# Performance work log

Measured on AMD Instinct MI355X. Metric: run time of the kernel, lower is better.

Reference implementation:

```python
import jax, jax.numpy as jnp
import numpy as np

QLEN, BSZ, D_MODEL = 2048, 4, 1024
N_HEAD, D_HEAD = 16, 64
SCALE = 1.0 / D_HEAD ** 0.5


def _rope(t, cos, sin):
    # t: [len, b, n, d_head]; cos/sin: [len, d_head//2]
    tr = t.reshape(*t.shape[:-1], D_HEAD // 2, 2)
    t_r, t_i = tr[..., 0], tr[..., 1]
    c = cos[:, None, None, :]
    s = sin[:, None, None, :]
    o_r = t_r * c - t_i * s
    o_i = t_r * s + t_i * c
    return jnp.stack([o_r, o_i], axis=-1).reshape(t.shape)


def setup_inputs() -> dict:
    key = jax.random.key(0)
    ks = jax.random.split(key, 9)
    x = jax.random.normal(ks[0], (QLEN, BSZ, D_MODEL), dtype=jnp.float32)
    # standard RoPE frequencies: theta = 10000^{-2i/d_head}
    inv_freq = 1.0 / (10000.0 ** (np.arange(0, D_HEAD, 2, dtype=np.float32) / D_HEAD))
    ang = np.arange(QLEN, dtype=np.float32)[:, None] * inv_freq[None, :]
    freqs_cos = jnp.asarray(np.cos(ang))
    freqs_sin = jnp.asarray(np.sin(ang))
    init = lambda k, sh: (jax.random.normal(k, sh, dtype=jnp.float32) * 0.02)
    H = N_HEAD * D_HEAD
    return {
        "x": x,
        "freqs_cos": freqs_cos,
        "freqs_sin": freqs_sin,
        "Wq": init(ks[1], (D_MODEL, H)), "bq": jnp.zeros((H,), jnp.float32),
        "Wk": init(ks[2], (D_MODEL, H)), "bk": jnp.zeros((H,), jnp.float32),
        "Wv": init(ks[3], (D_MODEL, H)), "bv": jnp.zeros((H,), jnp.float32),
        "Wo": init(ks[4], (H, D_MODEL)), "bo": jnp.zeros((D_MODEL,), jnp.float32),
    }


def reference(x, freqs_cos, freqs_sin, Wq, bq, Wk, bk, Wv, bv, Wo, bo):
    qlen, bsz, _ = x.shape
    q = x @ Wq + bq  # [q, b, n*d]
    k = x @ Wk + bk
    v = x @ Wv + bv
    new_mem = (k, v)
    q = q.reshape(qlen, bsz, N_HEAD, D_HEAD)
    k = k.reshape(qlen, bsz, N_HEAD, D_HEAD)
    vv = v.reshape(qlen, bsz, N_HEAD, D_HEAD)
    q = _rope(q, freqs_cos, freqs_sin)
    k = _rope(k, freqs_cos, freqs_sin)
    attn = jnp.einsum('ibnd,jbnd->ijbn', q, k) * SCALE
    p = jax.nn.softmax(attn, axis=1)
    o = jnp.einsum('ijbn,jbnd->ibnd', p, vv)
    o = o.reshape(qlen, bsz, N_HEAD * D_HEAD) @ Wo + bo
    return (o, new_mem[0], new_mem[1])
```

## Files before the change

kernel.cpp:

```cpp
#include <hip/hip_runtime.h>

typedef __attribute__((ext_vector_type(4))) float f32x4;
typedef __attribute__((ext_vector_type(16))) float f32x16;
typedef __attribute__((ext_vector_type(8))) __bf16 bf16x8;
typedef __attribute__((ext_vector_type(4))) __bf16 bf16x4;
typedef __attribute__((ext_vector_type(2))) __bf16 bf16x2;
typedef __attribute__((ext_vector_type(8))) unsigned short ushort8;
typedef __attribute__((ext_vector_type(4))) unsigned int u32x4;

#define DEVI __device__ __forceinline__

static constexpr int QLEN = 2048, BSZ = 4, DM = 1024, NH = 16, DH = 64;
static constexpr int MROWS = QLEN * BSZ;
static constexpr long OSZ  = (long)MROWS * DM;
static constexpr float SCL2E = 0.125f * 1.4426950408889634f;
static constexpr float RAW_THR = 4.0f / SCL2E;

DEVI void gload_lds16(const void* g, void* l) {
  __builtin_amdgcn_global_load_lds(
      (__attribute__((address_space(1))) void*)(size_t)g,
      (__attribute__((address_space(3))) void*)l, 16, 0, 0);
}

DEVI f32x16 zero16() {
  f32x16 v;
#pragma unroll
  for (int i = 0; i < 16; ++i) v[i] = 0.f;
  return v;
}

DEVI unsigned pack_bf16(float lo, float hi) {
  bf16x2 v = { (__bf16)lo, (__bf16)hi };
  return __builtin_bit_cast(unsigned, v);
}

__global__ void k_f32_to_bf16(const float* __restrict__ in, __bf16* __restrict__ out, int n4) {
  int i = blockIdx.x * blockDim.x + threadIdx.x;
  int stride = gridDim.x * blockDim.x;
  for (; i < n4; i += stride) {
    const float4 v = ((const float4*)in)[i];
    bf16x4 o = { (__bf16)v.x, (__bf16)v.y, (__bf16)v.z, (__bf16)v.w };
    ((bf16x4*)out)[i] = o;
  }
}

__global__ void k_wtrans(const float* __restrict__ W, __bf16* __restrict__ Wt) {
  __shared__ float tile[64][65];
  const int tk = blockIdx.x >> 4;
  const int tn = blockIdx.x & 15;
  const int t = threadIdx.x;
  const int r = t >> 4;
  const int c4 = (t & 15) << 2;
#pragma unroll
  for (int i = 0; i < 4; ++i) {
    const float4 v = *(const float4*)&W[(size_t)(tk * 64 + r + i * 16) * DM + tn * 64 + c4];
    tile[r + i * 16][c4 + 0] = v.x;
    tile[r + i * 16][c4 + 1] = v.y;
    tile[r + i * 16][c4 + 2] = v.z;
    tile[r + i * 16][c4 + 3] = v.w;
  }
  __syncthreads();
#pragma unroll
  for (int i = 0; i < 4; ++i) {
    const int n = r + i * 16;
    bf16x4 o = { (__bf16)tile[c4 + 0][n], (__bf16)tile[c4 + 1][n],
                 (__bf16)tile[c4 + 2][n], (__bf16)tile[c4 + 3][n] };
    *(bf16x4*)&Wt[(size_t)(tn * 64 + n) * DM + tk * 64 + c4] = o;
  }
}

DEVI void gemm_tile_core(const __bf16* __restrict__ A, const __bf16* __restrict__ Bt,
                         char* Alds, char* Blds, int m0, int n0, int t,
                         f32x4 (&acc)[4][4]) {
  constexpr int K = 1024;
  const int l = t & 63;
  const int w = t >> 6;
  const int wr = w >> 1, wc = w & 1;

  int a_addr[2][4], b_addr[2][4];
#pragma unroll
  for (int s = 0; s < 2; ++s)
#pragma unroll
    for (int f = 0; f < 4; ++f) {
      const int ca = s * 64 + ((l >> 4) << 4);
      const int ra = wr * 64 + f * 16 + (l & 15);
      a_addr[s][f] = ra * 128 + (ca ^ ((ra & 7) << 4));
      const int rb = wc * 64 + f * 16 + (l & 15);
      b_addr[s][f] = rb * 128 + (ca ^ ((rb & 7) << 4));
    }

  int g_row[4], g_col[4];
#pragma unroll
  for (int i = 0; i < 4; ++i) {
    const int g = i * 256 + t;
    g_row[i] = g >> 3;
    g_col[i] = ((g & 7) ^ (g_row[i] & 7)) * 8;
  }

  for (int kt = 0; kt < K / 64; ++kt) {
#pragma unroll
    for (int i = 0; i < 4; ++i) {
      gload_lds16(A + (size_t)(m0 + g_row[i]) * K + kt * 64 + g_col[i],
                  Alds + (size_t)(i * 256 + t) * 16);
      gload_lds16(Bt + (size_t)(n0 + g_row[i]) * K + kt * 64 + g_col[i],
                  Blds + (size_t)(i * 256 + t) * 16);
    }
    __syncthreads();
#pragma unroll
    for (int s = 0; s < 2; ++s) {
      bf16x8 af[4], bfr[4];
#pragma unroll
      for (int f = 0; f < 4; ++f) {
        af[f]  = *(const bf16x8*)(Alds + a_addr[s][f]);
        bfr[f] = *(const bf16x8*)(Blds + b_addr[s][f]);
      }
#pragma unroll
      for (int mi = 0; mi < 4; ++mi)
#pragma unroll
        for (int ni = 0; ni < 4; ++ni)
          acc[mi][ni] = __builtin_amdgcn_mfma_f32_16x16x32_bf16(af[mi], bfr[ni], acc[mi][ni], 0, 0, 0);
    }
    __syncthreads();
  }
}

__global__ __launch_bounds__(256, 2) void k_gemm(
    const __bf16* __restrict__ A, const __bf16* __restrict__ Bt,
    const float* __restrict__ bias, float* __restrict__ Cf, __bf16* __restrict__ Cb) {
  __shared__ alignas(16) char lds[32768];
  const int t = threadIdx.x;
  const int l = t & 63;
  const int w = t >> 6;
  const int n0 = (blockIdx.x & 7) * 128;
  const int m0 = (blockIdx.x >> 3) * 128;
  const int wr = w >> 1, wc = w & 1;

  f32x4 acc[4][4];
#pragma unroll
  for (int i = 0; i < 4; ++i)
#pragma unroll
    for (int j = 0; j < 4; ++j) acc[i][j] = (f32x4){0.f, 0.f, 0.f, 0.f};

  gemm_tile_core(A, Bt, lds, lds + 16384, m0, n0, t, acc);

  const int rowb = m0 + wr * 64 + ((l >> 4) << 2);
  const int colb = n0 + wc * 64 + (l & 15);
#pragma unroll
  for (int ni = 0; ni < 4; ++ni) {
    const float bv = bias[colb + ni * 16];
#pragma unroll
    for (int mi = 0; mi < 4; ++mi)
#pragma unroll
      for (int r = 0; r < 4; ++r) {
        const float v = acc[mi][ni][r] + bv;
        const size_t idx = (size_t)(rowb + mi * 16 + r) * 1024 + colb + ni * 16;
        Cf[idx] = v;
        if (Cb) Cb[idx] = (__bf16)v;
      }
  }
}

__global__ __launch_bounds__(256, 2) void k_gemm_qkv(
    const __bf16* __restrict__ A, const __bf16* __restrict__ Bt,
    const float* __restrict__ bq, const float* __restrict__ bk, const float* __restrict__ bv,
    float* __restrict__ oq, float* __restrict__ ok, float* __restrict__ ov,
    __bf16* __restrict__ vb) {
  __shared__ alignas(16) char lds[32768];
  const int t = threadIdx.x;
  const int l = t & 63;
  const int w = t >> 6;
  const int nt = blockIdx.x % 24;
  const int n0 = nt * 128;
  const int m0 = (blockIdx.x / 24) * 128;
  const int wr = w >> 1, wc = w & 1;

  f32x4 acc[4][4];
#pragma unroll
  for (int i = 0; i < 4; ++i)
#pragma unroll
    for (int j = 0; j < 4; ++j) acc[i][j] = (f32x4){0.f, 0.f, 0.f, 0.f};

  gemm_tile_core(A, Bt, lds, lds + 16384, m0, n0, t, acc);

  const int grp = n0 >> 10;
  const float* bias = grp == 0 ? bq : (grp == 1 ? bk : bv);
  float* Cf = grp == 0 ? oq : (grp == 1 ? ok : ov);
  __bf16* Cb = grp == 2 ? vb : nullptr;

  const int rowb = m0 + wr * 64 + ((l >> 4) << 2);
  const int colb = (n0 & 1023) + wc * 64 + (l & 15);
#pragma unroll
  for (int ni = 0; ni < 4; ++ni) {
    const float bvv = bias[colb + ni * 16];
#pragma unroll
    for (int mi = 0; mi < 4; ++mi)
#pragma unroll
      for (int r = 0; r < 4; ++r) {
        const float v = acc[mi][ni][r] + bvv;
        const size_t idx = (size_t)(rowb + mi * 16 + r) * 1024 + colb + ni * 16;
        Cf[idx] = v;
        if (Cb) Cb[idx] = (__bf16)v;
      }
  }
}

__global__ void k_rope(const float* __restrict__ qf, const float* __restrict__ kf,
                       const float* __restrict__ fc, const float* __restrict__ fs,
                       __bf16* __restrict__ qr, __bf16* __restrict__ kr) {
  const int i = blockIdx.x * blockDim.x + threadIdx.x;
  const int m = i >> 8;
  const int cp2 = i & 255;
  const int s = m >> 2;
  const int p2 = cp2 & 15;
  const float2 c2 = *(const float2*)&fc[s * 32 + p2 * 2];
  const float2 s2 = *(const float2*)&fs[s * 32 + p2 * 2];
  const float4 q4 = ((const float4*)qf)[i];
  const float4 k4 = ((const float4*)kf)[i];
  bf16x4 qo = { (__bf16)(q4.x * c2.x - q4.y * s2.x), (__bf16)(q4.x * s2.x + q4.y * c2.x),
                (__bf16)(q4.z * c2.y - q4.w * s2.y), (__bf16)(q4.z * s2.y + q4.w * c2.y) };
  bf16x4 ko = { (__bf16)(k4.x * c2.x - k4.y * s2.x), (__bf16)(k4.x * s2.x + k4.y * c2.x),
                (__bf16)(k4.z * c2.y - k4.w * s2.y), (__bf16)(k4.z * s2.y + k4.w * c2.y) };
  ((bf16x4*)qr)[i] = qo;
  ((bf16x4*)kr)[i] = ko;
}

static constexpr int KSLAB = 8192;
static constexpr int VSLAB_STRIDE = 1040;
static constexpr int VSLAB = 8 * VSLAB_STRIDE;
static constexpr int FBUF = KSLAB + VSLAB;

__global__ __launch_bounds__(256, 4) void k_flash3(
    const __bf16* __restrict__ Q, const __bf16* __restrict__ Kr,
    const __bf16* __restrict__ V, __bf16* __restrict__ O) {
  __shared__ alignas(16) char lds[2 * FBUF];

  const int t = threadIdx.x, l = t & 63, w = t >> 6;
  const int hf = l >> 5;
  const int q32 = l & 31;
  const int bid = blockIdx.x;
  const int qt = bid & 15;
  const int bh = bid >> 4;
  const int b = bh >> 4, hd = bh & 15;

  const int qrow = qt * 128 + w * 32 + q32;

  bf16x8 qf[4];
#pragma unroll
  for (int kc = 0; kc < 4; ++kc)
    qf[kc] = *(const bf16x8*)(Q + (size_t)(qrow * 4 + b) * DM + hd * 64 + kc * 16 + hf * 8);

  f32x16 acc0 = zero16(), acc1 = zero16();
  float m_run = -3.0e38f, l_run = 0.f;

  const int ksrc_j = t & 31;
  const int ksrc_d = (t >> 5) * 8;

  const int vj0 = (t & 31) * 2;
  const int vd0 = (t >> 5) * 8;
  const int vt_wbase = ((((t & 31) >> 3) * 2 + (t >> 7)) * VSLAB_STRIDE)
                     + (((((t & 31) >> 2) & 1) * 32 + (((t >> 5) & 3) * 8)) * 16)
                     + (((t & 31) & 3) * 4);

  {
    char* Kl = lds;
#pragma unroll
    for (int i = 0; i < 2; ++i)
      gload_lds16(Kr + (size_t)(((0 * 64) + i * 32 + ksrc_j) * 4 + b) * DM + hd * 64 + ksrc_d,
                  Kl + (size_t)(i * 256 + t) * 16);
    const __bf16* vsrc = V + (size_t)((0 * 64 + vj0) * 4 + b) * DM + hd * 64 + vd0;
    const ushort8 r0 = *(const ushort8*)vsrc;
    const ushort8 r1 = *(const ushort8*)(vsrc + 4 * DM);
    char* Vl = lds + KSLAB;
#pragma unroll
    for (int e = 0; e < 8; ++e) {
      const unsigned pack = (unsigned)r0[e] | ((unsigned)r1[e] << 16);
      *(unsigned*)(Vl + vt_wbase + e * 16) = pack;
    }
  }

  for (int kt = 0; kt < QLEN / 64; ++kt) {
    const int cur = kt & 1;
    char* Kl = lds + cur * FBUF;
    char* Vl = Kl + KSLAB;
    char* Kn = lds + (cur ^ 1) * FBUF;
    char* Vn = Kn + KSLAB;

    __syncthreads();

    ushort8 vr0, vr1;
    const bool have_next = (kt + 1) < QLEN / 64;
    if (have_next) {
#pragma unroll
      for (int i = 0; i < 2; ++i)
        gload_lds16(Kr + (size_t)((((kt + 1) * 64) + i * 32 + ksrc_j) * 4 + b) * DM + hd * 64 + ksrc_d,
                    Kn + (size_t)(i * 256 + t) * 16);
      const __bf16* vsrc = V + (size_t)(((kt + 1) * 64 + vj0) * 4 + b) * DM + hd * 64 + vd0;
      vr0 = *(const ushort8*)vsrc;
      vr1 = *(const ushort8*)(vsrc + 4 * DM);
    }

#pragma unroll
    for (int c = 0; c < 2; ++c) {
      f32x16 sc = zero16();
#pragma unroll
      for (int kc = 0; kc < 4; ++kc) {
        const bf16x8 kf = *(const bf16x8*)(Kl + (c * 4 + kc) * 1024 + l * 16);
        sc = __builtin_amdgcn_mfma_f32_32x32x16_bf16(kf, qf[kc], sc, 0, 0, 0);
      }

      float red[8];
#pragma unroll
      for (int i = 0; i < 8; ++i) red[i] = fmaxf(sc[i], sc[i + 8]);
#pragma unroll
      for (int i = 0; i < 4; ++i) red[i] = fmaxf(red[i], red[i + 4]);
      float pmax = fmaxf(fmaxf(red[0], red[2]), fmaxf(red[1], red[3]));
      pmax = fmaxf(pmax, __shfl_xor(pmax, 32));

      if (!__all(pmax - m_run <= RAW_THR)) {
        const float mn = fmaxf(m_run, pmax);
        const float alpha = __builtin_amdgcn_exp2f((m_run - mn) * SCL2E);
        l_run *= alpha;
        acc0 = acc0 * alpha;
        acc1 = acc1 * alpha;
        m_run = mn;
      }

#pragma unroll
      for (int r = 0; r < 16; ++r) sc[r] = __builtin_amdgcn_exp2f((sc[r] - m_run) * SCL2E);
      float sred[8];
#pragma unroll
      for (int i = 0; i < 8; ++i) sred[i] = sc[i] + sc[i + 8];
#pragma unroll
      for (int i = 0; i < 4; ++i) sred[i] = sred[i] + sred[i + 4];
      float rs = (sred[0] + sred[2]) + (sred[1] + sred[3]);
      rs += __shfl_xor(rs, 32);
      l_run += rs;

      unsigned pk[8];
#pragma unroll
      for (int m = 0; m < 4; ++m)
#pragma unroll
        for (int i = 0; i < 2; ++i)
          pk[m * 2 + i] = pack_bf16(sc[4 * m + 2 * i], sc[4 * m + 2 * i + 1]);

#pragma unroll
      for (int jc2 = 0; jc2 < 2; ++jc2) {
        unsigned w0 = pk[4 * jc2 + 0], w2 = pk[4 * jc2 + 2];
        unsigned w1 = pk[4 * jc2 + 1], w3 = pk[4 * jc2 + 3];
        asm("v_permlane32_swap_b32 %0, %1" : "+v"(w0), "+v"(w2));
        asm("v_permlane32_swap_b32 %0, %1" : "+v"(w1), "+v"(w3));
        const u32x4 pw = { w0, w1, w2, w3 };
        const bf16x8 pf = __builtin_bit_cast(bf16x8, pw);
        const int jc = c * 2 + jc2;
        {
          const bf16x8 vf = *(const bf16x8*)(Vl + (jc * 2 + 0) * VSLAB_STRIDE + l * 16);
          acc0 = __builtin_amdgcn_mfma_f32_32x32x16_bf16(vf, pf, acc0, 0, 0, 0);
        }
        {
          const bf16x8 vf = *(const bf16x8*)(Vl + (jc * 2 + 1) * VSLAB_STRIDE + l * 16);
          acc1 = __builtin_amdgcn_mfma_f32_32x32x16_bf16(vf, pf, acc1, 0, 0, 0);
        }
      }
    }

    if (have_next) {
#pragma unroll
      for (int e = 0; e < 8; ++e) {
        const unsigned pack = (unsigned)vr0[e] | ((unsigned)vr1[e] << 16);
        *(unsigned*)(Vn + vt_wbase + e * 16) = pack;
      }
    }
  }

  const float inv = 1.0f / l_run;
#pragma unroll
  for (int g = 0; g < 4; ++g) {
    {
      const int d0 = 0 * 32 + 8 * g + 4 * hf;
      bf16x4 o4 = { (__bf16)(acc0[4 * g + 0] * inv), (__bf16)(acc0[4 * g + 1] * inv),
                    (__bf16)(acc0[4 * g + 2] * inv), (__bf16)(acc0[4 * g + 3] * inv) };
      *(bf16x4*)&O[(size_t)(qrow * 4 + b) * DM + hd * 64 + d0] = o4;
    }
    {
      const int d0 = 1 * 32 + 8 * g + 4 * hf;
      bf16x4 o4 = { (__bf16)(acc1[4 * g + 0] * inv), (__bf16)(acc1[4 * g + 1] * inv),
                    (__bf16)(acc1[4 * g + 2] * inv), (__bf16)(acc1[4 * g + 3] * inv) };
      *(bf16x4*)&O[(size_t)(qrow * 4 + b) * DM + hd * 64 + d0] = o4;
    }
  }
}

extern "C" void kernel_launch(void* const* d_in, const int* in_sizes, int n_in,
                              void* d_out, int out_size, void* d_ws, size_t ws_size,
                              hipStream_t stream) {
  const float* x    = (const float*)d_in[0];
  const float* fcos = (const float*)d_in[1];
  const float* fsin = (const float*)d_in[2];
  const float* Wq   = (const float*)d_in[3];
  const float* bq   = (const float*)d_in[4];
  const float* Wk   = (const float*)d_in[5];
  const float* bk   = (const float*)d_in[6];
  const float* Wv   = (const float*)d_in[7];
  const float* bv   = (const float*)d_in[8];
  const float* Wo   = (const float*)d_in[9];
  const float* bo   = (const float*)d_in[10];

  float* out_o = (float*)d_out;
  float* out_k = out_o + OSZ;
  float* out_v = out_o + 2 * OSZ;

  char* ws = (char*)d_ws;
  __bf16* xb  = (__bf16*)(ws);
  __bf16* wqt = (__bf16*)(ws + 16777216);
  __bf16* wkt = (__bf16*)(ws + 18874368);
  __bf16* wvt = (__bf16*)(ws + 20971520);
  __bf16* wot = (__bf16*)(ws + 23068672);
  __bf16* qr  = (__bf16*)(ws + 25165824);
  __bf16* kr  = (__bf16*)(ws + 41943040);
  __bf16* vb  = (__bf16*)(ws + 58720256);
  __bf16* ao  = (__bf16*)(ws + 75497472);

  k_f32_to_bf16<<<2048, 256, 0, stream>>>(x, xb, (int)(OSZ / 4));
  k_wtrans<<<256, 256, 0, stream>>>(Wq, wqt);
  k_wtrans<<<256, 256, 0, stream>>>(Wk, wkt);
  k_wtrans<<<256, 256, 0, stream>>>(Wv, wvt);
  k_wtrans<<<256, 256, 0, stream>>>(Wo, wot);

  k_gemm_qkv<<<1536, 256, 0, stream>>>(xb, wqt, bq, bk, bv, out_o, out_k, out_v, vb);

  k_rope<<<8192, 256, 0, stream>>>(out_o, out_k, fcos, fsin, qr, kr);

  k_flash3<<<1024, 256, 0, stream>>>(qr, kr, vb, ao);

  k_gemm<<<512, 256, 0, stream>>>(ao, wot, bo, out_o, (__bf16*)nullptr);
}
```

Before: 226.8 us.

## Fuse RoPE into QKV GEMM epilogue, pre-transpose V, add MFMA priority hints

RoPE is now applied in the QKV GEMM epilogue using a lane shuffle to fetch the paired element. This removes the separate rope kernel and the fp32 Q round trip through the output buffer. A new kernel transposes V into a per-head [d, seq] layout, reusing the xb workspace, so the flash kernel reads V fragments straight from global memory instead of staging transposed tiles in LDS. The change also adds s_setprio around MFMA blocks, a swizzled block order, and a cheaper max reduction. In exchange it adds an extra launch and V pass, and flash now issues uncached global V loads inside the loop.

Result: slower. 276.8 us (+22.1%).

```diff
diff --git a/kernel.cpp b/kernel.cpp
--- a/kernel.cpp
+++ b/kernel.cpp
@@ -69,6 +69,33 @@
   }
 }
 
+__global__ __launch_bounds__(256, 4) void k_vtrans(const __bf16* __restrict__ vb,
+                                                   __bf16* __restrict__ VT) {
+  __shared__ __bf16 tile[128][66];
+  const int t = threadIdx.x;
+  const int bh = blockIdx.x >> 4;
+  const int s0 = (blockIdx.x & 15) * 128;
+  const int b = bh >> 4, h = bh & 15;
+  const int sl = t >> 4;
+  const int d4 = (t & 15) * 4;
+#pragma unroll
+  for (int it = 0; it < 8; ++it) {
+    const int s = sl + it * 16;
+    *(bf16x4*)&tile[s][d4] = *(const bf16x4*)&vb[(size_t)((s0 + s) * 4 + b) * DM + h * 64 + d4];
+  }
+  __syncthreads();
+  const int d = t >> 2;
+  const int sp = t & 3;
+#pragma unroll
+  for (int j = 0; j < 4; ++j) {
+    const int sb = sp * 32 + j * 8;
+    bf16x8 pk;
+#pragma unroll
+    for (int i = 0; i < 8; ++i) pk[i] = tile[sb + i][d];
+    *(bf16x8*)&VT[(size_t)(bh * 64 + d) * QLEN + s0 + sb] = pk;
+  }
+}
+
 DEVI void gemm_tile_core(const __bf16* __restrict__ A, const __bf16* __restrict__ Bt,
                          char* Alds, char* Blds, int m0, int n0, int t,
                          f32x4 (&acc)[4][4]) {
@@ -114,11 +141,13 @@
         af[f]  = *(const bf16x8*)(Alds + a_addr[s][f]);
         bfr[f] = *(const bf16x8*)(Blds + b_addr[s][f]);
       }
+      __builtin_amdgcn_s_setprio(1);
 #pragma unroll
       for (int mi = 0; mi < 4; ++mi)
 #pragma unroll
         for (int ni = 0; ni < 4; ++ni)
           acc[mi][ni] = __builtin_amdgcn_mfma_f32_16x16x32_bf16(af[mi], bfr[ni], acc[mi][ni], 0, 0, 0);
+      __builtin_amdgcn_s_setprio(0);
     }
     __syncthreads();
   }
@@ -126,7 +155,7 @@
 
 __global__ __launch_bounds__(256, 2) void k_gemm(
     const __bf16* __restrict__ A, const __bf16* __restrict__ Bt,
-    const float* __restrict__ bias, float* __restrict__ Cf, __bf16* __restrict__ Cb) {
+    const float* __restrict__ bias, float* __restrict__ Cf) {
   __shared__ alignas(16) char lds[32768];
   const int t = threadIdx.x;
   const int l = t & 63;
@@ -151,20 +180,17 @@
 #pragma unroll
     for (int mi = 0; mi < 4; ++mi)
 #pragma unroll
-      for (int r = 0; r < 4; ++r) {
-        const float v = acc[mi][ni][r] + bv;
-        const size_t idx = (size_t)(rowb + mi * 16 + r) * 1024 + colb + ni * 16;
-        Cf[idx] = v;
-        if (Cb) Cb[idx] = (__bf16)v;
-      }
+      for (int r = 0; r < 4; ++r)
+        Cf[(size_t)(rowb + mi * 16 + r) * 1024 + colb + ni * 16] = acc[mi][ni][r] + bv;
   }
 }
 
 __global__ __launch_bounds__(256, 2) void k_gemm_qkv(
     const __bf16* __restrict__ A, const __bf16* __restrict__ Bt,
     const float* __restrict__ bq, const float* __restrict__ bk, const float* __restrict__ bv,
-    float* __restrict__ oq, float* __restrict__ ok, float* __restrict__ ov,
-    __bf16* __restrict__ vb) {
+    const float* __restrict__ fc, const float* __restrict__ fs,
+    float* __restrict__ ok, float* __restrict__ ov,
+    __bf16* __restrict__ qr, __bf16* __restrict__ kr, __bf16* __restrict__ vb) {
   __shared__ alignas(16) char lds[32768];
   const int t = threadIdx.x;
   const int l = t & 63;
@@ -183,63 +209,62 @@
   gemm_tile_core(A, Bt, lds, lds + 16384, m0, n0, t, acc);
 
   const int grp = n0 >> 10;
-  const float* bias = grp == 0 ? bq : (grp == 1 ? bk : bv);
-  float* Cf = grp == 0 ? oq : (grp == 1 ? ok : ov);
-  __bf16* Cb = grp == 2 ? vb : nullptr;
-
   const int rowb = m0 + wr * 64 + ((l >> 4) << 2);
   const int colb = (n0 & 1023) + wc * 64 + (l & 15);
-#pragma unroll
-  for (int ni = 0; ni < 4; ++ni) {
-    const float bvv = bias[colb + ni * 16];
-#pragma unroll
-    for (int mi = 0; mi < 4; ++mi)
-#pragma unroll
-      for (int r = 0; r < 4; ++r) {
-        const float v = acc[mi][ni][r] + bvv;
-        const size_t idx = (size_t)(rowb + mi * 16 + r) * 1024 + colb + ni * 16;
-        Cf[idx] = v;
-        if (Cb) Cb[idx] = (__bf16)v;
+
+  if (grp == 2) {
+#pragma unroll
+    for (int ni = 0; ni < 4; ++ni) {
+      const float bvv = bv[colb + ni * 16];
+#pragma unroll
+      for (int mi = 0; mi < 4; ++mi)
+#pragma unroll
+        for (int r = 0; r < 4; ++r) {
+          const float v = acc[mi][ni][r] + bvv;
+          const size_t idx = (size_t)(rowb + mi * 16 + r) * 1024 + colb + ni * 16;
+          ov[idx] = v;
+          vb[idx] = (__bf16)v;
+        }
+    }
+  } else {
+    const float* bias = grp == 0 ? bq : bk;
+    __bf16* Rb = grp == 0 ? qr : kr;
+    const float sgn = (l & 1) ? 1.f : -1.f;
+#pragma unroll
+    for (int ni = 0; ni < 4; ++ni) {
+      const int col = colb + ni * 16;
+      const float bvv = bias[col];
+      const int p = (col & 63) >> 1;
+#pragma unroll
+      for (int mi = 0; mi < 4; ++mi) {
+        const int s_idx = (rowb + mi * 16) >> 2;
+        const float cv = fc[s_idx * 32 + p];
+        const float sv = fs[s_idx * 32 + p] * sgn;
+#pragma unroll
+        for (int r = 0; r < 4; ++r) {
+          const float v = acc[mi][ni][r] + bvv;
+          if (grp == 1) ok[(size_t)(rowb + mi * 16 + r) * 1024 + col] = v;
+          const float part = __shfl_xor(v, 1);
+          Rb[(size_t)(rowb + mi * 16 + r) * 1024 + col] = (__bf16)(v * cv + part * sv);
+        }
       }
-  }
-}
-
-__global__ void k_rope(const float* __restrict__ qf, const float* __restrict__ kf,
-                       const float* __restrict__ fc, const float* __restrict__ fs,
-                       __bf16* __restrict__ qr, __bf16* __restrict__ kr) {
-  const int i = blockIdx.x * blockDim.x + threadIdx.x;
-  const int m = i >> 8;
-  const int cp2 = i & 255;
-  const int s = m >> 2;
-  const int p2 = cp2 & 15;
-  const float2 c2 = *(const float2*)&fc[s * 32 + p2 * 2];
-  const float2 s2 = *(const float2*)&fs[s * 32 + p2 * 2];
-  const float4 q4 = ((const float4*)qf)[i];
-  const float4 k4 = ((const float4*)kf)[i];
-  bf16x4 qo = { (__bf16)(q4.x * c2.x - q4.y * s2.x), (__bf16)(q4.x * s2.x + q4.y * c2.x),
-                (__bf16)(q4.z * c2.y - q4.w * s2.y), (__bf16)(q4.z * s2.y + q4.w * c2.y) };
-  bf16x4 ko = { (__bf16)(k4.x * c2.x - k4.y * s2.x), (__bf16)(k4.x * s2.x + k4.y * c2.x),
-                (__bf16)(k4.z * c2.y - k4.w * s2.y), (__bf16)(k4.z * s2.y + k4.w * c2.y) };
-  ((bf16x4*)qr)[i] = qo;
-  ((bf16x4*)kr)[i] = ko;
-}
-
-static constexpr int KSLAB = 8192;
-static constexpr int VSLAB_STRIDE = 1040;
-static constexpr int VSLAB = 8 * VSLAB_STRIDE;
-static constexpr int FBUF = KSLAB + VSLAB;
-
-__global__ __launch_bounds__(256, 4) void k_flash3(
+    }
+  }
+}
+
+static constexpr int KSLAB4 = 8192;
+
+__global__ __launch_bounds__(256, 4) void k_flash4(
     const __bf16* __restrict__ Q, const __bf16* __restrict__ Kr,
-    const __bf16* __restrict__ V, __bf16* __restrict__ O) {
-  __shared__ alignas(16) char lds[2 * FBUF];
+    const __bf16* __restrict__ VT, __bf16* __restrict__ O) {
+  __shared__ alignas(16) char lds[2 * KSLAB4];
 
   const int t = threadIdx.x, l = t & 63, w = t >> 6;
   const int hf = l >> 5;
   const int q32 = l & 31;
-  const int bid = blockIdx.x;
-  const int qt = bid & 15;
-  const int bh = bid >> 4;
+  const int swz = (blockIdx.x & 7) * 128 + (blockIdx.x >> 3);
+  const int qt = swz & 15;
+  const int bh = swz >> 4;
   const int b = bh >> 4, hd = bh & 15;
 
   const int qrow = qt * 128 + w * 32 + q32;
@@ -254,66 +279,51 @@
 
   const int ksrc_j = t & 31;
   const int ksrc_d = (t >> 5) * 8;
-
-  const int vj0 = (t & 31) * 2;
-  const int vd0 = (t >> 5) * 8;
-  const int vt_wbase = ((((t & 31) >> 3) * 2 + (t >> 7)) * VSLAB_STRIDE)
-                     + (((((t & 31) >> 2) & 1) * 32 + (((t >> 5) & 3) * 8)) * 16)
-                     + (((t & 31) & 3) * 4);
-
-  {
-    char* Kl = lds;
-#pragma unroll
-    for (int i = 0; i < 2; ++i)
-      gload_lds16(Kr + (size_t)(((0 * 64) + i * 32 + ksrc_j) * 4 + b) * DM + hd * 64 + ksrc_d,
-                  Kl + (size_t)(i * 256 + t) * 16);
-    const __bf16* vsrc = V + (size_t)((0 * 64 + vj0) * 4 + b) * DM + hd * 64 + vd0;
-    const ushort8 r0 = *(const ushort8*)vsrc;
-    const ushort8 r1 = *(const ushort8*)(vsrc + 4 * DM);
-    char* Vl = lds + KSLAB;
-#pragma unroll
-    for (int e = 0; e < 8; ++e) {
-      const unsigned pack = (unsigned)r0[e] | ((unsigned)r1[e] << 16);
-      *(unsigned*)(Vl + vt_wbase + e * 16) = pack;
-    }
-  }
+  const __bf16* vbase = VT + (size_t)(bh * 64 + q32) * QLEN + hf * 8;
+
+#pragma unroll
+  for (int i = 0; i < 2; ++i)
+    gload_lds16(Kr + (size_t)((i * 32 + ksrc_j) * 4 + b) * DM + hd * 64 + ksrc_d,
+                lds + (size_t)(i * 256 + t) * 16);
 
   for (int kt = 0; kt < QLEN / 64; ++kt) {
     const int cur = kt & 1;
-    char* Kl = lds + cur * FBUF;
-    char* Vl = Kl + KSLAB;
-    char* Kn = lds + (cur ^ 1) * FBUF;
-    char* Vn = Kn + KSLAB;
+    char* Kl = lds + cur * KSLAB4;
+    char* Kn = lds + (cur ^ 1) * KSLAB4;
 
     __syncthreads();
 
-    ushort8 vr0, vr1;
-    const bool have_next = (kt + 1) < QLEN / 64;
-    if (have_next) {
+    if (kt + 1 < QLEN / 64) {
 #pragma unroll
       for (int i = 0; i < 2; ++i)
         gload_lds16(Kr + (size_t)((((kt + 1) * 64) + i * 32 + ksrc_j) * 4 + b) * DM + hd * 64 + ksrc_d,
                     Kn + (size_t)(i * 256 + t) * 16);
-      const __bf16* vsrc = V + (size_t)(((kt + 1) * 64 + vj0) * 4 + b) * DM + hd * 64 + vd0;
-      vr0 = *(const ushort8*)vsrc;
-      vr1 = *(const ushort8*)(vsrc + 4 * DM);
     }
 
 #pragma unroll
     for (int c = 0; c < 2; ++c) {
+      bf16x8 vf00 = *(const bf16x8*)(vbase + (size_t)0 * 32 * QLEN + kt * 64 + (c * 2 + 0) * 16);
+      bf16x8 vf01 = *(const bf16x8*)(vbase + (size_t)1 * 32 * QLEN + kt * 64 + (c * 2 + 0) * 16);
+      bf16x8 vf10 = *(const bf16x8*)(vbase + (size_t)0 * 32 * QLEN + kt * 64 + (c * 2 + 1) * 16);
+      bf16x8 vf11 = *(const bf16x8*)(vbase + (size_t)1 * 32 * QLEN + kt * 64 + (c * 2 + 1) * 16);
+
       f32x16 sc = zero16();
+      __builtin_amdgcn_s_setprio(1);
 #pragma unroll
       for (int kc = 0; kc < 4; ++kc) {
         const bf16x8 kf = *(const bf16x8*)(Kl + (c * 4 + kc) * 1024 + l * 16);
         sc = __builtin_amdgcn_mfma_f32_32x32x16_bf16(kf, qf[kc], sc, 0, 0, 0);
       }
-
-      float red[8];
-#pragma unroll
-      for (int i = 0; i < 8; ++i) red[i] = fmaxf(sc[i], sc[i + 8]);
-#pragma unroll
-      for (int i = 0; i < 4; ++i) red[i] = fmaxf(red[i], red[i + 4]);
-      float pmax = fmaxf(fmaxf(red[0], red[2]), fmaxf(red[1], red[3]));
+      __builtin_amdgcn_s_setprio(0);
+
+      const float a0 = fmaxf(fmaxf(sc[0], sc[1]), sc[2]);
+      const float a1 = fmaxf(fmaxf(sc[3], sc[4]), sc[5]);
+      const float a2 = fmaxf(fmaxf(sc[6], sc[7]), sc[8]);
+      const float a3 = fmaxf(fmaxf(sc[9], sc[10]), sc[11]);
+      const float a4 = fmaxf(fmaxf(sc[12], sc[13]), sc[14]);
+      const float b0 = fmaxf(fmaxf(a0, a1), a2);
+      const float b1 = fmaxf(fmaxf(a3, a4), sc[15]);
+      float pmax = fmaxf(b0, b1);
       pmax = fmaxf(pmax, __shfl_xor(pmax, 32));
 
       if (!__all(pmax - m_run <= RAW_THR)) {
@@ -351,23 +361,15 @@
         asm("v_permlane32_swap_b32 %0, %1" : "+v"(w1), "+v"(w3));
         const u32x4 pw = { w0, w1, w2, w3 };
         const bf16x8 pf = __builtin_bit_cast(bf16x8, pw);
-        const int jc = c * 2 + jc2;
-        {
-          const bf16x8 vf = *(const bf16x8*)(Vl + (jc * 2 + 0) * VSLAB_STRIDE + l * 16);
-          acc0 = __builtin_amdgcn_mfma_f32_32x32x16_bf16(vf, pf, acc0, 0, 0, 0);
+        __builtin_amdgcn_s_setprio(1);
+        if (jc2 == 0) {
+          acc0 = __builtin_amdgcn_mfma_f32_32x32x16_bf16(vf00, pf, acc0, 0, 0, 0);
+          acc1 = __builtin_amdgcn_mfma_f32_32x32x16_bf16(vf01, pf, acc1, 0, 0, 0);
+        } else {
+          acc0 = __builtin_amdgcn_mfma_f32_32x32x16_bf16(vf10, pf, acc0, 0, 0, 0);
+          acc1 = __builtin_amdgcn_mfma_f32_32x32x16_bf16(vf11, pf, acc1, 0, 0, 0);
         }
-        {
-          const bf16x8 vf = *(const bf16x8*)(Vl + (jc * 2 + 1) * VSLAB_STRIDE + l * 16);
-          acc1 = __builtin_amdgcn_mfma_f32_32x32x16_bf16(vf, pf, acc1, 0, 0, 0);
-        }
-      }
-    }
-
-    if (have_next) {
-#pragma unroll
-      for (int e = 0; e < 8; ++e) {
-        const unsigned pack = (unsigned)vr0[e] | ((unsigned)vr1[e] << 16);
-        *(unsigned*)(Vn + vt_wbase + e * 16) = pack;
+        __builtin_amdgcn_s_setprio(0);
       }
     }
   }
@@ -376,13 +378,13 @@
 #pragma unroll
   for (int g = 0; g < 4; ++g) {
     {
-      const int d0 = 0 * 32 + 8 * g + 4 * hf;
+      const int d0 = 8 * g + 4 * hf;
       bf16x4 o4 = { (__bf16)(acc0[4 * g + 0] * inv), (__bf16)(acc0[4 * g + 1] * inv),
                     (__bf16)(acc0[4 * g + 2] * inv), (__bf16)(acc0[4 * g + 3] * inv) };
       *(bf16x4*)&O[(size_t)(qrow * 4 + b) * DM + hd * 64 + d0] = o4;
     }
     {
-      const int d0 = 1 * 32 + 8 * g + 4 * hf;
+      const int d0 = 32 + 8 * g + 4 * hf;
       bf16x4 o4 = { (__bf16)(acc1[4 * g + 0] * inv), (__bf16)(acc1[4 * g + 1] * inv),
                     (__bf16)(acc1[4 * g + 2] * inv), (__bf16)(acc1[4 * g + 3] * inv) };
       *(bf16x4*)&O[(size_t)(qrow * 4 + b) * DM + hd * 64 + d0] = o4;
@@ -411,6 +413,7 @@
 
   char* ws = (char*)d_ws;
   __bf16* xb  = (__bf16*)(ws);
+  __bf16* VT  = (__bf16*)(ws);
   __bf16* wqt = (__bf16*)(ws + 16777216);
   __bf16* wkt = (__bf16*)(ws + 18874368);
   __bf16* wvt = (__bf16*)(ws + 20971520);
@@ -426,11 +429,12 @@
   k_wtrans<<<256, 256, 0, stream>>>(Wv, wvt);
   k_wtrans<<<256, 256, 0, stream>>>(Wo, wot);
 
-  k_gemm_qkv<<<1536, 256, 0, stream>>>(xb, wqt, bq, bk, bv, out_o, out_k, out_v, vb);
-
-  k_rope<<<8192, 256, 0, stream>>>(out_o, out_k, fcos, fsin, qr, kr);
-
-  k_flash3<<<1024, 256, 0, stream>>>(qr, kr, vb, ao);
-
-  k_gemm<<<512, 256, 0, stream>>>(ao, wot, bo, out_o, (__bf16*)nullptr);
-}
+  k_gemm_qkv<<<1536, 256, 0, stream>>>(xb, wqt, bq, bk, bv, fcos, fsin,
+                                       out_k, out_v, qr, kr, vb);
+
+  k_vtrans<<<1024, 256, 0, stream>>>(vb, VT);
+
+  k_flash4<<<1024, 256, 0, stream>>>(qr, kr, VT, ao);
+
+  k_gemm<<<512, 256, 0, stream>>>(ao, wot, bo, out_o);
+}
```
